# Performance work log

Measured on AMD Instinct MI355X. Metric: run time of the kernel, lower is better.

Reference implementation:

```python
import jax, jax.numpy as jnp
import numpy as np

N_NODES = 50000
N_REL = 3
N_EDGES = 500000
D_IN, D_HID, D_OUT = 128, 256, 128


def setup_inputs() -> dict:
    key = jax.random.key(0)
    ks = jax.random.split(key, 9)
    def w(k, shape, fan_in):
        return jax.random.normal(k, shape, dtype=jnp.float32) / np.sqrt(fan_in)
    return {
        "x": jax.random.normal(ks[0], (N_NODES, D_IN), dtype=jnp.float32),
        "src": jax.random.randint(ks[1], (N_REL, N_EDGES), 0, N_NODES, dtype=jnp.int32),
        "dst": jax.random.randint(ks[2], (N_REL, N_EDGES), 0, N_NODES, dtype=jnp.int32),
        "w_self1": w(ks[3], (N_REL, D_IN, D_HID), D_IN),
        "w_neigh1": w(ks[4], (N_REL, D_IN, D_HID), D_IN),
        "b1": jnp.zeros((N_REL, D_HID), dtype=jnp.float32),
        "w_self2": w(ks[5], (N_REL, D_HID, D_OUT), D_HID),
        "w_neigh2": w(ks[6], (N_REL, D_HID, D_OUT), D_HID),
        "b2": jnp.zeros((N_REL, D_OUT), dtype=jnp.float32),
    }


def _sage_hetero_layer(x, src, dst, w_self, w_neigh, b):
    """Multi-relation SAGEConv (mean agg); relation outputs summed (HeteroGraphConv default).
    x: [N, din]; src/dst: [R, E]; w_*: [R, din, dout]; b: [R, dout]."""
    n = x.shape[0]

    def per_rel(s, d, ws, wn, bb):
        gathered = jnp.take(x, s, axis=0)                      # [E, din] neighbor gather
        summed = jax.ops.segment_sum(gathered, d, num_segments=n)  # [N, din]
        deg = jax.ops.segment_sum(jnp.ones(s.shape, jnp.float32), d, num_segments=n)
        h_neigh = summed / jnp.maximum(deg, 1.0)[:, None]      # mean, 0 for isolated dst
        return x @ ws + h_neigh @ wn + bb                      # fc_self + fc_neigh + bias

    per_rel_out = jax.vmap(per_rel)(src, dst, w_self, w_neigh, b)  # [R, N, dout]
    return per_rel_out.sum(axis=0)


def reference(x, src, dst, w_self1, w_neigh1, b1, w_self2, w_neigh2, b2):
    h = _sage_hetero_layer(x, src, dst, w_self1, w_neigh1, b1)
    h = jax.nn.relu(h)  # SAGEConv activation in hidden layers
    out = _sage_hetero_layer(h, src, dst, w_self2, w_neigh2, b2)  # last layer: no activation
    return out
```

## Files before the change

### kernel.cpp

```cpp
#include <hip/hip_runtime.h>

#define NN 50000
#define NREL 3
#define NE 500000
#define DIN 128
#define DHID 256
#define DOUT 128

#define NBUK 98
#define CAP 8192
#define EPB 2048
#define NCHK ((NE + EPB - 1) / EPB)

typedef unsigned int uint;
typedef unsigned short ushort;
typedef __attribute__((ext_vector_type(8))) short bf16x8;
typedef __attribute__((ext_vector_type(4))) float f32x4;

using gptr_t = const __attribute__((address_space(1))) unsigned int*;
using lptr_t = __attribute__((address_space(3))) unsigned int*;

__device__ __forceinline__ ushort f2bf(float f) {
    uint u = __float_as_uint(f);
    uint r = (u + 0x7fffu + ((u >> 16) & 1u)) >> 16;
    return (ushort)r;
}
__device__ __forceinline__ void acc2(float2& a, uint u) {
    a.x += __uint_as_float(u << 16);
    a.y += __uint_as_float(u & 0xffff0000u);
}

__global__ __launch_bounds__(256) void pass_a(const int* __restrict__ src,
                                              const int* __restrict__ dst,
                                              int* __restrict__ bcursor,
                                              uint* __restrict__ pairs) {
    int r = blockIdx.x / NCHK;
    int chunk = blockIdx.x % NCHK;
    int e0 = chunk * EPB;
    int nedge = min(EPB, NE - e0);
    const int* S = src + (size_t)r * NE + e0;
    const int* D = dst + (size_t)r * NE + e0;
    __shared__ int cnt[NBUK], base[NBUK], cur[NBUK];
    int tid = threadIdx.x;
    if (tid < NBUK) { cnt[tid] = 0; cur[tid] = 0; }
    __syncthreads();
    uint pk[8];
    int bk[8];
    bool val[8];
#pragma unroll
    for (int j = 0; j < 8; ++j) {
        int e = j * 256 + tid;
        val[j] = e < nedge;
        int d = val[j] ? D[e] : 0;
        int s = val[j] ? S[e] : 0;
        bk[j] = d >> 9;
        pk[j] = ((uint)s << 9) | (uint)(d & 511);
        if (val[j]) atomicAdd(&cnt[bk[j]], 1);
    }
    __syncthreads();
    if (tid < NBUK) base[tid] = atomicAdd(&bcursor[r * NBUK + tid], cnt[tid]);
    __syncthreads();
#pragma unroll
    for (int j = 0; j < 8; ++j) {
        if (val[j]) {
            int slot = base[bk[j]] + atomicAdd(&cur[bk[j]], 1);
            if (slot < CAP) pairs[(size_t)(r * NBUK + bk[j]) * CAP + slot] = pk[j];
        }
    }
}

__global__ __launch_bounds__(256) void pass_b(const uint* __restrict__ pairs,
                                              const int* __restrict__ bcnt,
                                              int* __restrict__ srclist,
                                              int* __restrict__ deg,
                                              int* __restrict__ offs) {
    int blk = blockIdx.x;
    int b = blk % NBUK;
    int r = blk / NBUK;
    int node_base = b * 512;
    int count = min(bcnt[blk], CAP);
    int obase = blk * CAP;
    const uint* pp = pairs + (size_t)blk * CAP;
    __shared__ int hist[512];
    __shared__ int cur[512];
    __shared__ int sc[256];
    int tid = threadIdx.x;
    hist[tid] = 0;
    hist[tid + 256] = 0;
    __syncthreads();
    for (int i = tid; i < count; i += 256) atomicAdd(&hist[pp[i] & 511], 1);
    __syncthreads();
    int v0 = hist[2 * tid], v1 = hist[2 * tid + 1];
    int s = v0 + v1;
    sc[tid] = s;
    __syncthreads();
    for (int st = 1; st < 256; st <<= 1) {
        int t = (tid >= st) ? sc[tid - st] : 0;
        __syncthreads();
        sc[tid] += t;
        __syncthreads();
    }
    int excl = sc[tid] - s;
    int c0 = obase + excl;
    int c1 = c0 + v0;
    cur[2 * tid] = c0;
    cur[2 * tid + 1] = c1;
    int n0 = node_base + 2 * tid;
    if (n0 < NN)     { deg[r * NN + n0] = v0;     offs[r * NN + n0] = c0; }
    if (n0 + 1 < NN) { deg[r * NN + n0 + 1] = v1; offs[r * NN + n0 + 1] = c1; }
    __syncthreads();
    for (int i = tid; i < count; i += 256) {
        uint p = pp[i];
        int pos = atomicAdd(&cur[p & 511], 1);
        srclist[pos] = (int)(p >> 9);
    }
}

#define F2B_BLKS 6250
__global__ __launch_bounds__(256) void prep_kernel(
    const float* __restrict__ x, ushort* __restrict__ xb,
    const float* __restrict__ ws1, const float* __restrict__ wn1, ushort* __restrict__ Bt1,
    const float* __restrict__ ws2, const float* __restrict__ wn2, ushort* __restrict__ Bt2,
    const float* __restrict__ b1, float* __restrict__ bsum1,
    const float* __restrict__ b2, float* __restrict__ bsum2) {
    int blk = blockIdx.x, tid = threadIdx.x;
    if (blk < F2B_BLKS) {
        int t = blk * 256 + tid;
        float4 v = *(const float4*)(x + (size_t)t * 4);
        uint2 p;
        p.x = (uint)f2bf(v.x) | ((uint)f2bf(v.y) << 16);
        p.y = (uint)f2bf(v.z) | ((uint)f2bf(v.w) << 16);
        *(uint2*)(xb + (size_t)t * 4) = p;
    } else if (blk < F2B_BLKS + 512) {
        int t = (blk - F2B_BLKS) * 256 + tid;
        int n = t >> 9, k = t & 511;
        int b = k >> 7, kk = k & 127;
        float v;
        if (b == 0)
            v = ws1[kk * 256 + n] + ws1[128 * 256 + kk * 256 + n] + ws1[2 * 128 * 256 + kk * 256 + n];
        else
            v = wn1[(size_t)(b - 1) * 128 * 256 + kk * 256 + n];
        Bt1[t] = f2bf(v);
    } else if (blk < F2B_BLKS + 1024) {
        int t = (blk - F2B_BLKS - 512) * 256 + tid;
        int n = t >> 8, k = t & 255;
        int c = n >> 7, j = n & 127;
        float v;
        if (c == 0)
            v = ws2[k * 128 + j] + ws2[256 * 128 + k * 128 + j] + ws2[2 * 256 * 128 + k * 128 + j];
        else
            v = wn2[(size_t)(c - 1) * 256 * 128 + k * 128 + j];
        Bt2[t] = f2bf(v);
    } else {
        if (tid < DHID) bsum1[tid] = b1[tid] + b1[DHID + tid] + b1[2 * DHID + tid];
        if (tid < DOUT) bsum2[tid] = b2[tid] + b2[DOUT + tid] + b2[2 * DOUT + tid];
    }
}

template <int PHASE>
__global__ __launch_bounds__(256) void gather3(
    const ushort* __restrict__ f0, const ushort* __restrict__ f1,
    const ushort* __restrict__ f2, const int* __restrict__ offs,
    const int* __restrict__ deg, const int* __restrict__ srclist,
    ushort* __restrict__ ob, float* __restrict__ of) {
    int node = blockIdx.x * 4 + (threadIdx.x >> 6);
    if (node >= NN) return;
    int lane = threadIdx.x & 63;
    int g = lane >> 4, c = lane & 15;
    float2 msum[4];
#pragma unroll
    for (int k = 0; k < 4; ++k) msum[k] = make_float2(0.f, 0.f);

    for (int r = 0; r < NREL; ++r) {
        const ushort* feat = (r == 0) ? f0 : (r == 1) ? f1 : f2;
        int beg = offs[r * NN + node];
        int d = deg[r * NN + node];
        float2 ac[4];
#pragma unroll
        for (int k = 0; k < 4; ++k) ac[k] = make_float2(0.f, 0.f);

        for (int i0 = 0; i0 < d; i0 += 64) {
            int m = d - i0;
            if (m > 64) m = 64;
            int sid_l = (lane < m) ? srclist[beg + i0 + lane] : 0;
            for (int j0 = 0; j0 < m; j0 += 8) {
                int j1 = j0 + g;
                int j2 = j0 + 4 + g;
                int s1 = __shfl(sid_l, (j1 < m) ? j1 : 0);
                int s2 = __shfl(sid_l, (j2 < m) ? j2 : 0);
                uint4 v1 = *(const uint4*)(feat + (size_t)s1 * 128 + c * 8);
                uint4 v2 = *(const uint4*)(feat + (size_t)s2 * 128 + c * 8);
                if (j1 < m) {
                    acc2(ac[0], v1.x); acc2(ac[1], v1.y);
                    acc2(ac[2], v1.z); acc2(ac[3], v1.w);
                }
                if (j2 < m) {
                    acc2(ac[0], v2.x); acc2(ac[1], v2.y);
                    acc2(ac[2], v2.z); acc2(ac[3], v2.w);
                }
            }
        }
#pragma unroll
        for (int k = 0; k < 4; ++k) {
            ac[k].x += __shfl_xor(ac[k].x, 16);
            ac[k].y += __shfl_xor(ac[k].y, 16);
            ac[k].x += __shfl_xor(ac[k].x, 32);
            ac[k].y += __shfl_xor(ac[k].y, 32);
        }
        float inv = 1.f / fmaxf((float)d, 1.f);
        if (PHASE == 0) {
            if (g == 0) {
                uint4 pk;
                pk.x = (uint)f2bf(ac[0].x * inv) | ((uint)f2bf(ac[0].y * inv) << 16);
                pk.y = (uint)f2bf(ac[1].x * inv) | ((uint)f2bf(ac[1].y * inv) << 16);
                pk.z = (uint)f2bf(ac[2].x * inv) | ((uint)f2bf(ac[2].y * inv) << 16);
                pk.w = (uint)f2bf(ac[3].x * inv) | ((uint)f2bf(ac[3].y * inv) << 16);
                *(uint4*)(ob + (size_t)r * NN * DIN + (size_t)node * 128 + c * 8) = pk;
            }
        } else {
#pragma unroll
            for (int k = 0; k < 4; ++k) {
                msum[k].x += ac[k].x * inv;
                msum[k].y += ac[k].y * inv;
            }
        }
    }
    if (PHASE == 1 && g == 0) {
        float* po = of + (size_t)node * 128 + c * 8;
        float4 a = *(float4*)po;
        float4 b = *(float4*)(po + 4);
        a.x += msum[0].x; a.y += msum[0].y; a.z += msum[1].x; a.w += msum[1].y;
        b.x += msum[2].x; b.y += msum[2].y; b.z += msum[3].x; b.w += msum[3].y;
        *(float4*)po = a;
        *(float4*)(po + 4) = b;
    }
}

template <int LAYER>
__global__ __launch_bounds__(512) void gemm_mfma(
    const ushort* __restrict__ A0, const ushort* __restrict__ A1,
    const ushort* __restrict__ A2, const ushort* __restrict__ A3,
    const ushort* __restrict__ Bt, const float* __restrict__ bias,
    ushort* __restrict__ HO, float* __restrict__ CO,
    ushort* __restrict__ Y1, ushort* __restrict__ Y2, ushort* __restrict__ Y3) {
    constexpr int KTOT = (LAYER == 1) ? 512 : 256;
    constexpr int ASTRIDE = (LAYER == 1) ? 128 : 256;
    __shared__ __align__(16) ushort As[128 * 32];
    __shared__ __align__(16) ushort Bs[256 * 32];

    const int tid = threadIdx.x, lane = tid & 63, w = tid >> 6;
    const int wr = w >> 2, wc = w & 3;
    const int bm = blockIdx.x * 128;
    const int bn = blockIdx.y * 256;

    f32x4 acc[4][4];
#pragma unroll
    for (int m = 0; m < 4; ++m)
#pragma unroll
        for (int n = 0; n < 4; ++n) acc[m][n] = (f32x4){0.f, 0.f, 0.f, 0.f};

    const int srow = tid >> 2;
    const int schunk = (tid & 3) * 8;

    for (int k0 = 0; k0 < KTOT; k0 += 32) {
        const ushort* Ab = A0;
        int koff = k0;
        if (LAYER == 1) {
            int b = k0 >> 7;
            Ab = (b == 0) ? A0 : (b == 1) ? A1 : (b == 2) ? A2 : A3;
            koff = k0 & 127;
        }
        {
            const ushort* srcA = Ab + (size_t)(bm + srow) * ASTRIDE + koff + schunk;
            __builtin_amdgcn_global_load_lds((gptr_t)srcA, (lptr_t)(As + w * 512), 16, 0, 0);
        }
#pragma unroll
        for (int i = 0; i < 2; ++i) {
            int row = i * 128 + srow;
            const ushort* srcB = Bt + (size_t)(bn + row) * KTOT + k0 + schunk;
            __builtin_amdgcn_global_load_lds((gptr_t)srcB, (lptr_t)(Bs + i * 4096 + w * 512), 16, 0, 0);
        }
        __syncthreads();

        const int r = lane & 15, g = lane >> 4;
        bf16x8 af[4], bg[4];
#pragma unroll
        for (int m = 0; m < 4; ++m)
            af[m] = *(const bf16x8*)&As[(wr * 64 + m * 16 + r) * 32 + g * 8];
#pragma unroll
        for (int n = 0; n < 4; ++n)
            bg[n] = *(const bf16x8*)&Bs[(wc * 64 + n * 16 + r) * 32 + g * 8];
#pragma unroll
        for (int m = 0; m < 4; ++m)
#pragma unroll
            for (int n = 0; n < 4; ++n)
                acc[m][n] = __builtin_amdgcn_mfma_f32_16x16x32_bf16(af[m], bg[n], acc[m][n], 0, 0, 0);
        __syncthreads();
    }

    const int r = lane & 15, g = lane >> 4;
    if (LAYER == 1) {
#pragma unroll
        for (int m = 0; m < 4; ++m)
#pragma unroll
            for (int v = 0; v < 4; ++v) {
                int gm = bm + wr * 64 + m * 16 + g * 4 + v;
                if (gm >= NN) continue;
#pragma unroll
                for (int n = 0; n < 4; ++n) {
                    int gn = wc * 64 + n * 16 + r;
                    float f = acc[m][n][v] + bias[gn];
                    f = fmaxf(f, 0.f);
                    HO[(size_t)gm * 256 + gn] = f2bf(f);
                }
            }
    } else {
        int buf = (bn >> 7) + (wc >> 1);
        ushort* Y = (buf == 1) ? Y1 : (buf == 2) ? Y2 : Y3;
#pragma unroll
        for (int m = 0; m < 4; ++m)
#pragma unroll
            for (int v = 0; v < 4; ++v) {
                int gm = bm + wr * 64 + m * 16 + g * 4 + v;
                if (gm >= NN) continue;
#pragma unroll
                for (int n = 0; n < 4; ++n) {
                    int col = (wc & 1) * 64 + n * 16 + r;
                    if (buf == 0)
                        CO[(size_t)gm * 128 + col] = acc[m][n][v] + bias[col];
                    else
                        Y[(size_t)gm * 128 + col] = f2bf(acc[m][n][v]);
                }
            }
    }
}

extern "C" void kernel_launch(void* const* d_in, const int* in_sizes, int n_in,
                              void* d_out, int out_size, void* d_ws, size_t ws_size,
                              hipStream_t stream) {
    const float* x        = (const float*)d_in[0];
    const int*   src      = (const int*)d_in[1];
    const int*   dst      = (const int*)d_in[2];
    const float* w_self1  = (const float*)d_in[3];
    const float* w_neigh1 = (const float*)d_in[4];
    const float* b1       = (const float*)d_in[5];
    const float* w_self2  = (const float*)d_in[6];
    const float* w_neigh2 = (const float*)d_in[7];
    const float* b2       = (const float*)d_in[8];
    float* out = (float*)d_out;

    char* ws = (char*)d_ws;
    size_t off = 0;
    auto alloc = [&](size_t bytes) {
        char* p = ws + off;
        off += (bytes + 255) & ~(size_t)255;
        return p;
    };
    int*    bcursor = (int*)alloc(NREL * NBUK * 4);
    int*    deg     = (int*)alloc(NREL * NN * 4);
    int*    offs    = (int*)alloc(NREL * NN * 4);
    int*    srclist = (int*)alloc((size_t)NREL * NBUK * CAP * 4);
    float*  bsum1   = (float*)alloc(DHID * 4);
    float*  bsum2   = (float*)alloc(DOUT * 4);
    ushort* Bt1     = (ushort*)alloc((size_t)DHID * 512 * 2);
    ushort* Bt2     = (ushort*)alloc((size_t)512 * DHID * 2);
    ushort* xb      = (ushort*)alloc((size_t)NN * DIN * 2);
    ushort* aggb    = (ushort*)alloc((size_t)NREL * NN * DIN * 2);
    ushort* Hb      = (ushort*)alloc((size_t)NN * DHID * 2);
    (void)alloc(65536);
    uint* pairs = (uint*)Hb;

    hipMemsetAsync(bcursor, 0, NREL * NBUK * 4, stream);
    pass_a<<<NREL * NCHK, 256, 0, stream>>>(src, dst, bcursor, pairs);
    pass_b<<<NREL * NBUK, 256, 0, stream>>>(pairs, bcursor, srclist, deg, offs);

    prep_kernel<<<F2B_BLKS + 1024 + 1, 256, 0, stream>>>(
        x, xb, w_self1, w_neigh1, Bt1, w_self2, w_neigh2, Bt2, b1, bsum1, b2, bsum2);

    int ggrid = (NN + 3) / 4;

    gather3<0><<<ggrid, 256, 0, stream>>>(xb, xb, xb, offs, deg, srclist, aggb, nullptr);
    {
        dim3 grid((NN + 127) / 128, 1);
        gemm_mfma<1><<<grid, 512, 0, stream>>>(
            xb, aggb, aggb + (size_t)NN * DIN, aggb + (size_t)2 * NN * DIN,
            Bt1, bsum1, Hb, nullptr, nullptr, nullptr, nullptr);
    }
    {
        dim3 grid((NN + 127) / 128, 2);
        gemm_mfma<2><<<grid, 512, 0, stream>>>(
            Hb, nullptr, nullptr, nullptr, Bt2, bsum2,
            nullptr, out, aggb, aggb + (size_t)NN * DIN, aggb + (size_t)2 * NN * DIN);
    }
    gather3<1><<<ggrid, 256, 0, stream>>>(
        aggb, aggb + (size_t)NN * DIN, aggb + (size_t)2 * NN * DIN,
        offs, deg, srclist, nullptr, out);
}
```

Measured before the change: 243.7 us.

## Pad neighbor lists to multiples of eight with zero row, fuse bucketing with prep

Each node's CSR segment is padded to a multiple of 8 entries, and the padding points at an added all-zero feature row. This lets the gather loop drop its per-edge bounds checks and predication. Source ids are stored as pre-scaled byte offsets, so the gather skips the multiply. The pass_a bucketing kernel is merged into the prep conversion kernel to remove one launch, and the feature buffers gain one extra zero row each. The cost is some wasted loads on padding and a larger srclist footprint, which must still fit within CAP.

```diff
diff --git a/kernel.cpp b/kernel.cpp
--- a/kernel.cpp
+++ b/kernel.cpp
@@ -11,6 +11,9 @@
 #define CAP 8192
 #define EPB 2048
 #define NCHK ((NE + EPB - 1) / EPB)
+#define PA_BLKS (NREL * NCHK)
+#define F2B_BLKS 6250
+#define ZROW ((uint)NN << 8)
 
 typedef unsigned int uint;
 typedef unsigned short ushort;
@@ -30,100 +33,52 @@
     a.y += __uint_as_float(u & 0xffff0000u);
 }
 
-__global__ __launch_bounds__(256) void pass_a(const int* __restrict__ src,
-                                              const int* __restrict__ dst,
-                                              int* __restrict__ bcursor,
-                                              uint* __restrict__ pairs) {
-    int r = blockIdx.x / NCHK;
-    int chunk = blockIdx.x % NCHK;
-    int e0 = chunk * EPB;
-    int nedge = min(EPB, NE - e0);
-    const int* S = src + (size_t)r * NE + e0;
-    const int* D = dst + (size_t)r * NE + e0;
-    __shared__ int cnt[NBUK], base[NBUK], cur[NBUK];
-    int tid = threadIdx.x;
-    if (tid < NBUK) { cnt[tid] = 0; cur[tid] = 0; }
-    __syncthreads();
-    uint pk[8];
-    int bk[8];
-    bool val[8];
-#pragma unroll
-    for (int j = 0; j < 8; ++j) {
-        int e = j * 256 + tid;
-        val[j] = e < nedge;
-        int d = val[j] ? D[e] : 0;
-        int s = val[j] ? S[e] : 0;
-        bk[j] = d >> 9;
-        pk[j] = ((uint)s << 9) | (uint)(d & 511);
-        if (val[j]) atomicAdd(&cnt[bk[j]], 1);
-    }
-    __syncthreads();
-    if (tid < NBUK) base[tid] = atomicAdd(&bcursor[r * NBUK + tid], cnt[tid]);
-    __syncthreads();
-#pragma unroll
-    for (int j = 0; j < 8; ++j) {
-        if (val[j]) {
-            int slot = base[bk[j]] + atomicAdd(&cur[bk[j]], 1);
-            if (slot < CAP) pairs[(size_t)(r * NBUK + bk[j]) * CAP + slot] = pk[j];
-        }
-    }
-}
-
-__global__ __launch_bounds__(256) void pass_b(const uint* __restrict__ pairs,
-                                              const int* __restrict__ bcnt,
-                                              int* __restrict__ srclist,
-                                              int* __restrict__ deg,
-                                              int* __restrict__ offs) {
-    int blk = blockIdx.x;
-    int b = blk % NBUK;
-    int r = blk / NBUK;
-    int node_base = b * 512;
-    int count = min(bcnt[blk], CAP);
-    int obase = blk * CAP;
-    const uint* pp = pairs + (size_t)blk * CAP;
-    __shared__ int hist[512];
-    __shared__ int cur[512];
-    __shared__ int sc[256];
-    int tid = threadIdx.x;
-    hist[tid] = 0;
-    hist[tid + 256] = 0;
-    __syncthreads();
-    for (int i = tid; i < count; i += 256) atomicAdd(&hist[pp[i] & 511], 1);
-    __syncthreads();
-    int v0 = hist[2 * tid], v1 = hist[2 * tid + 1];
-    int s = v0 + v1;
-    sc[tid] = s;
-    __syncthreads();
-    for (int st = 1; st < 256; st <<= 1) {
-        int t = (tid >= st) ? sc[tid - st] : 0;
-        __syncthreads();
-        sc[tid] += t;
-        __syncthreads();
-    }
-    int excl = sc[tid] - s;
-    int c0 = obase + excl;
-    int c1 = c0 + v0;
-    cur[2 * tid] = c0;
-    cur[2 * tid + 1] = c1;
-    int n0 = node_base + 2 * tid;
-    if (n0 < NN)     { deg[r * NN + n0] = v0;     offs[r * NN + n0] = c0; }
-    if (n0 + 1 < NN) { deg[r * NN + n0 + 1] = v1; offs[r * NN + n0 + 1] = c1; }
-    __syncthreads();
-    for (int i = tid; i < count; i += 256) {
-        uint p = pp[i];
-        int pos = atomicAdd(&cur[p & 511], 1);
-        srclist[pos] = (int)(p >> 9);
-    }
-}
-
-#define F2B_BLKS 6250
-__global__ __launch_bounds__(256) void prep_kernel(
+__global__ __launch_bounds__(256) void pass_a_prep(
+    const int* __restrict__ src, const int* __restrict__ dst,
+    int* __restrict__ bcursor, uint* __restrict__ pairs,
     const float* __restrict__ x, ushort* __restrict__ xb,
     const float* __restrict__ ws1, const float* __restrict__ wn1, ushort* __restrict__ Bt1,
     const float* __restrict__ ws2, const float* __restrict__ wn2, ushort* __restrict__ Bt2,
     const float* __restrict__ b1, float* __restrict__ bsum1,
-    const float* __restrict__ b2, float* __restrict__ bsum2) {
+    const float* __restrict__ b2, float* __restrict__ bsum2,
+    ushort* __restrict__ agg0, ushort* __restrict__ agg1, ushort* __restrict__ agg2) {
     int blk = blockIdx.x, tid = threadIdx.x;
+    if (blk < PA_BLKS) {
+        int r = blk / NCHK;
+        int chunk = blk % NCHK;
+        int e0 = chunk * EPB;
+        int nedge = min(EPB, NE - e0);
+        const int* S = src + (size_t)r * NE + e0;
+        const int* D = dst + (size_t)r * NE + e0;
+        __shared__ int cnt[NBUK], base[NBUK], cur[NBUK];
+        if (tid < NBUK) { cnt[tid] = 0; cur[tid] = 0; }
+        __syncthreads();
+        uint pk[8];
+        int bk[8];
+        bool val[8];
+#pragma unroll
+        for (int j = 0; j < 8; ++j) {
+            int e = j * 256 + tid;
+            val[j] = e < nedge;
+            int d = val[j] ? D[e] : 0;
+            int s = val[j] ? S[e] : 0;
+            bk[j] = d >> 9;
+            pk[j] = ((uint)s << 9) | (uint)(d & 511);
+            if (val[j]) atomicAdd(&cnt[bk[j]], 1);
+        }
+        __syncthreads();
+        if (tid < NBUK) base[tid] = atomicAdd(&bcursor[r * NBUK + tid], cnt[tid]);
+        __syncthreads();
+#pragma unroll
+        for (int j = 0; j < 8; ++j) {
+            if (val[j]) {
+                int slot = base[bk[j]] + atomicAdd(&cur[bk[j]], 1);
+                if (slot < CAP) pairs[(size_t)(r * NBUK + bk[j]) * CAP + slot] = pk[j];
+            }
+        }
+        return;
+    }
+    blk -= PA_BLKS;
     if (blk < F2B_BLKS) {
         int t = blk * 256 + tid;
         float4 v = *(const float4*)(x + (size_t)t * 4);
@@ -154,50 +109,104 @@
     } else {
         if (tid < DHID) bsum1[tid] = b1[tid] + b1[DHID + tid] + b1[2 * DHID + tid];
         if (tid < DOUT) bsum2[tid] = b2[tid] + b2[DOUT + tid] + b2[2 * DOUT + tid];
-    }
+        if (tid >= 192 && tid < 256) {
+            int b = (tid - 192) >> 4, i = tid & 15;
+            ushort* row = (b == 0) ? xb : (b == 1) ? agg0 : (b == 2) ? agg1 : agg2;
+            uint4 z = {0u, 0u, 0u, 0u};
+            *(uint4*)(row + (size_t)NN * 128 + i * 8) = z;
+        }
+    }
+}
+
+__global__ __launch_bounds__(256) void pass_b(const uint* __restrict__ pairs,
+                                              const int* __restrict__ bcnt,
+                                              uint* __restrict__ srclist,
+                                              int* __restrict__ deg,
+                                              int* __restrict__ offs) {
+    int blk = blockIdx.x;
+    int b = blk % NBUK;
+    int r = blk / NBUK;
+    int node_base = b * 512;
+    int count = min(bcnt[blk], CAP);
+    int obase = blk * CAP;
+    const uint* pp = pairs + (size_t)blk * CAP;
+    __shared__ int hist[512];
+    __shared__ int cur[512];
+    __shared__ int sc[256];
+    int tid = threadIdx.x;
+    hist[tid] = 0;
+    hist[tid + 256] = 0;
+    __syncthreads();
+    for (int i = tid; i < count; i += 256) atomicAdd(&hist[pp[i] & 511], 1);
+    __syncthreads();
+    int v0 = hist[2 * tid], v1 = hist[2 * tid + 1];
+    int p0 = (v0 + 7) & ~7;
+    int p1 = (v1 + 7) & ~7;
+    int s = p0 + p1;
+    sc[tid] = s;
+    __syncthreads();
+    for (int st = 1; st < 256; st <<= 1) {
+        int t = (tid >= st) ? sc[tid - st] : 0;
+        __syncthreads();
+        sc[tid] += t;
+        __syncthreads();
+    }
+    int excl = sc[tid] - s;
+    int c0 = obase + excl;
+    int c1 = c0 + p0;
+    cur[2 * tid] = c0;
+    cur[2 * tid + 1] = c1;
+    int n0 = node_base + 2 * tid;
+    if (n0 < NN)     { deg[r * NN + n0] = v0;     offs[r * NN + n0] = c0; }
+    if (n0 + 1 < NN) { deg[r * NN + n0 + 1] = v1; offs[r * NN + n0 + 1] = c1; }
+    __syncthreads();
+    for (int i = tid; i < count; i += 256) {
+        uint p = pp[i];
+        int pos = atomicAdd(&cur[p & 511], 1);
+        srclist[pos] = (p >> 1) & ~255u;
+    }
+    __syncthreads();
+    for (int i = v0; i < p0; ++i) srclist[c0 + i] = ZROW;
+    for (int i = v1; i < p1; ++i) srclist[c1 + i] = ZROW;
 }
 
 template <int PHASE>
 __global__ __launch_bounds__(256) void gather3(
     const ushort* __restrict__ f0, const ushort* __restrict__ f1,
     const ushort* __restrict__ f2, const int* __restrict__ offs,
-    const int* __restrict__ deg, const int* __restrict__ srclist,
+    const int* __restrict__ deg, const uint* __restrict__ srclist,
     ushort* __restrict__ ob, float* __restrict__ of) {
     int node = blockIdx.x * 4 + (threadIdx.x >> 6);
     if (node >= NN) return;
     int lane = threadIdx.x & 63;
-    int g = lane >> 4, c = lane & 15;
+    int g = lane >> 4;
+    uint c16 = (uint)(lane & 15) * 16;
     float2 msum[4];
 #pragma unroll
     for (int k = 0; k < 4; ++k) msum[k] = make_float2(0.f, 0.f);
 
     for (int r = 0; r < NREL; ++r) {
-        const ushort* feat = (r == 0) ? f0 : (r == 1) ? f1 : f2;
+        const char* feat = (const char*)((r == 0) ? f0 : (r == 1) ? f1 : f2);
         int beg = offs[r * NN + node];
         int d = deg[r * NN + node];
+        int pd = (d + 7) & ~7;
         float2 ac[4];
 #pragma unroll
         for (int k = 0; k < 4; ++k) ac[k] = make_float2(0.f, 0.f);
 
-        for (int i0 = 0; i0 < d; i0 += 64) {
-            int m = d - i0;
-            if (m > 64) m = 64;
-            int sid_l = (lane < m) ? srclist[beg + i0 + lane] : 0;
-            for (int j0 = 0; j0 < m; j0 += 8) {
-                int j1 = j0 + g;
-                int j2 = j0 + 4 + g;
-                int s1 = __shfl(sid_l, (j1 < m) ? j1 : 0);
-                int s2 = __shfl(sid_l, (j2 < m) ? j2 : 0);
-                uint4 v1 = *(const uint4*)(feat + (size_t)s1 * 128 + c * 8);
-                uint4 v2 = *(const uint4*)(feat + (size_t)s2 * 128 + c * 8);
-                if (j1 < m) {
-                    acc2(ac[0], v1.x); acc2(ac[1], v1.y);
-                    acc2(ac[2], v1.z); acc2(ac[3], v1.w);
-                }
-                if (j2 < m) {
-                    acc2(ac[0], v2.x); acc2(ac[1], v2.y);
-                    acc2(ac[2], v2.z); acc2(ac[3], v2.w);
-                }
+        for (int i0 = 0; i0 < pd; i0 += 64) {
+            uint sid_l = srclist[beg + i0 + lane];
+            int lim = pd - i0;
+            if (lim > 64) lim = 64;
+            for (int j0 = 0; j0 < lim; j0 += 8) {
+                uint o1 = __shfl(sid_l, j0 + g) + c16;
+                uint o2 = __shfl(sid_l, j0 + 4 + g) + c16;
+                uint4 v1 = *(const uint4*)(feat + o1);
+                uint4 v2 = *(const uint4*)(feat + o2);
+                acc2(ac[0], v1.x); acc2(ac[1], v1.y);
+                acc2(ac[2], v1.z); acc2(ac[3], v1.w);
+                acc2(ac[0], v2.x); acc2(ac[1], v2.y);
+                acc2(ac[2], v2.z); acc2(ac[3], v2.w);
             }
         }
 #pragma unroll
@@ -215,7 +224,7 @@
                 pk.y = (uint)f2bf(ac[1].x * inv) | ((uint)f2bf(ac[1].y * inv) << 16);
                 pk.z = (uint)f2bf(ac[2].x * inv) | ((uint)f2bf(ac[2].y * inv) << 16);
                 pk.w = (uint)f2bf(ac[3].x * inv) | ((uint)f2bf(ac[3].y * inv) << 16);
-                *(uint4*)(ob + (size_t)r * NN * DIN + (size_t)node * 128 + c * 8) = pk;
+                *(uint4*)(ob + (size_t)r * (NN + 1) * DIN + (size_t)node * 128 + (c16 >> 1)) = pk;
             }
         } else {
 #pragma unroll
@@ -226,7 +235,7 @@
         }
     }
     if (PHASE == 1 && g == 0) {
-        float* po = of + (size_t)node * 128 + c * 8;
+        float* po = of + (size_t)node * 128 + (c16 >> 1);
         float4 a = *(float4*)po;
         float4 b = *(float4*)(po + 4);
         a.x += msum[0].x; a.y += msum[0].y; a.z += msum[1].x; a.w += msum[1].y;
@@ -356,26 +365,30 @@
         off += (bytes + 255) & ~(size_t)255;
         return p;
     };
+    const size_t NROW = NN + 1;
     int*    bcursor = (int*)alloc(NREL * NBUK * 4);
     int*    deg     = (int*)alloc(NREL * NN * 4);
     int*    offs    = (int*)alloc(NREL * NN * 4);
-    int*    srclist = (int*)alloc((size_t)NREL * NBUK * CAP * 4);
+    uint*   srclist = (uint*)alloc(((size_t)NREL * NBUK * CAP + 256) * 4);
     float*  bsum1   = (float*)alloc(DHID * 4);
     float*  bsum2   = (float*)alloc(DOUT * 4);
     ushort* Bt1     = (ushort*)alloc((size_t)DHID * 512 * 2);
     ushort* Bt2     = (ushort*)alloc((size_t)512 * DHID * 2);
-    ushort* xb      = (ushort*)alloc((size_t)NN * DIN * 2);
-    ushort* aggb    = (ushort*)alloc((size_t)NREL * NN * DIN * 2);
+    ushort* xb      = (ushort*)alloc(NROW * DIN * 2);
+    ushort* aggb    = (ushort*)alloc((size_t)NREL * NROW * DIN * 2);
     ushort* Hb      = (ushort*)alloc((size_t)NN * DHID * 2);
     (void)alloc(65536);
     uint* pairs = (uint*)Hb;
+    ushort* agg0 = aggb;
+    ushort* agg1 = aggb + NROW * DIN;
+    ushort* agg2 = aggb + 2 * NROW * DIN;
 
     hipMemsetAsync(bcursor, 0, NREL * NBUK * 4, stream);
-    pass_a<<<NREL * NCHK, 256, 0, stream>>>(src, dst, bcursor, pairs);
+    pass_a_prep<<<PA_BLKS + F2B_BLKS + 1024 + 1, 256, 0, stream>>>(
+        src, dst, bcursor, pairs,
+        x, xb, w_self1, w_neigh1, Bt1, w_self2, w_neigh2, Bt2,
+        b1, bsum1, b2, bsum2, agg0, agg1, agg2);
     pass_b<<<NREL * NBUK, 256, 0, stream>>>(pairs, bcursor, srclist, deg, offs);
-
-    prep_kernel<<<F2B_BLKS + 1024 + 1, 256, 0, stream>>>(
-        x, xb, w_self1, w_neigh1, Bt1, w_self2, w_neigh2, Bt2, b1, bsum1, b2, bsum2);
 
     int ggrid = (NN + 3) / 4;
 
@@ -383,16 +396,14 @@
     {
         dim3 grid((NN + 127) / 128, 1);
         gemm_mfma<1><<<grid, 512, 0, stream>>>(
-            xb, aggb, aggb + (size_t)NN * DIN, aggb + (size_t)2 * NN * DIN,
-            Bt1, bsum1, Hb, nullptr, nullptr, nullptr, nullptr);
+            xb, agg0, agg1, agg2, Bt1, bsum1, Hb, nullptr, nullptr, nullptr, nullptr);
     }
     {
         dim3 grid((NN + 127) / 128, 2);
         gemm_mfma<2><<<grid, 512, 0, stream>>>(
             Hb, nullptr, nullptr, nullptr, Bt2, bsum2,
-            nullptr, out, aggb, aggb + (size_t)NN * DIN, aggb + (size_t)2 * NN * DIN);
+            nullptr, out, agg0, agg1, agg2);
     }
     gather3<1><<<ggrid, 256, 0, stream>>>(
-        aggb, aggb + (size_t)NN * DIN, aggb + (size_t)2 * NN * DIN,
-        offs, deg, srclist, nullptr, out);
-}
+        agg0, agg1, agg2, offs, deg, srclist, nullptr, out);
+}
```

Measured after the change: 240.1 us. Within noise of the previous version (-1.5%).
